# Performance work log

Measured on AMD Instinct MI355X. Metric: run time of the kernel, lower is better.

Reference implementation:

```python
import jax, jax.numpy as jnp
import numpy as np

T = 5          # temporal_window_size
B = 512        # batch (graphs per timestep)
NA = 16        # num_agents (nodes per graph)
S = 64         # num_belief_states
A = 16         # action_dim
HID = 64       # hidden_dim per head
H = 4          # num_attn_heads
FD = HID * H   # 256, feature_dim
LAT = 128      # latent_dim
N = B * NA     # total nodes per timestep
FIN = S + A    # node feature dim
NEG_SLOPE = 0.2


def _edge_index():
    i, j = np.meshgrid(np.arange(NA), np.arange(NA), indexing='ij')
    m = i != j
    src_l, dst_l = i[m], j[m]                      # 240 intra-clique edges
    off = (np.arange(B) * NA)[:, None]
    src = (src_l[None] + off).ravel()
    dst = (dst_l[None] + off).ravel()
    loops = np.arange(N)                           # PyG GATConv add_self_loops=True
    src = np.concatenate([src, loops])
    dst = np.concatenate([dst, loops])
    return jnp.asarray(np.stack([src, dst]), dtype=jnp.int64)


def setup_inputs() -> dict:
    key = jax.random.key(0)
    ks = jax.random.split(key, 24)
    xav = lambda k, shp: jax.random.normal(k, shp, jnp.float32) * np.float32(np.sqrt(2.0 / (shp[0] + shp[-1])))
    return {
        'signals': jax.random.normal(ks[0], (T, B, S), jnp.float32),
        'neighbor_actions': jax.random.normal(ks[1], (T, B, NA * A), jnp.float32),
        'lin_w0': xav(ks[2], (FD, FIN)),
        'att_src0': xav(ks[3], (H, HID)),
        'att_dst0': xav(ks[4], (H, HID)),
        'bias0': jnp.zeros((FD,), jnp.float32),
        'lin_w1': xav(ks[5], (FD, FD)),
        'att_src1': xav(ks[6], (H, HID)),
        'att_dst1': xav(ks[7], (H, HID)),
        'bias1': jnp.zeros((FD,), jnp.float32),
        'in_proj_w': xav(ks[8], (3 * FD, FD)),
        'in_proj_b': jnp.zeros((3 * FD,), jnp.float32),
        'out_proj_w': xav(ks[9], (FD, FD)),
        'out_proj_b': jnp.zeros((FD,), jnp.float32),
        'w_mean': xav(ks[10], (LAT, FD)),
        'b_mean': jnp.zeros((LAT,), jnp.float32),
        'w_logvar': xav(ks[11], (LAT, FD)),
        'b_logvar': jnp.zeros((LAT,), jnp.float32),
        'w_belief': xav(ks[12], (S, FD)),
        'b_belief': jnp.zeros((S,), jnp.float32),
        'edge_index': _edge_index(),
    }


def _segment_softmax(e, seg, num_segments):
    # e: [E, T, H]; softmax over edges sharing the same target node.
    m = jax.ops.segment_max(e, seg, num_segments=num_segments)
    e = jnp.exp(e - m[seg])
    s = jax.ops.segment_sum(e, seg, num_segments=num_segments)
    return e / s[seg]


def _gat(x, src, dst, w, a_src, a_dst, b):
    # x: [N, T, Fin] -> [N, T, H*HID]   (PyG GATConv, concat heads)
    xl = jnp.einsum('ntf,of->nto', x, w).reshape(N, T, H, HID)
    e_src = jnp.einsum('nthc,hc->nth', xl, a_src)[src]   # [E, T, H]
    e_dst = jnp.einsum('nthc,hc->nth', xl, a_dst)[dst]
    e = jax.nn.leaky_relu(e_src + e_dst, NEG_SLOPE)
    alpha = _segment_softmax(e, dst, N)                  # per-target softmax
    out = jax.ops.segment_sum(alpha[..., None] * xl[src], dst, num_segments=N)
    return out.reshape(N, T, FD) + b


def reference(signals, neighbor_actions, lin_w0, att_src0, att_dst0, bias0,
              lin_w1, att_src1, att_dst1, bias1, in_proj_w, in_proj_b,
              out_proj_w, out_proj_b, w_mean, b_mean, w_logvar, b_logvar,
              w_belief, b_belief, edge_index):
    # --- _construct_graph (vectorized over time window + batch) ---
    acts = neighbor_actions.reshape(T, B, NA, A)
    beliefs = jnp.zeros((T, B, NA, S), signals.dtype).at[:, :, 0, :].set(signals)
    nodes = jnp.concatenate([beliefs, acts], -1).reshape(T, N, FIN)
    nodes = jnp.transpose(nodes, (1, 0, 2))              # [N, T, FIN]
    src, dst = edge_index[0], edge_index[1]
    x = jax.nn.relu(_gat(nodes, src, dst, lin_w0, att_src0, att_dst0, bias0))
    x = jax.nn.relu(_gat(x, src, dst, lin_w1, att_src1, att_dst1, bias1))
    # --- ego-node sequence: nodes 0, NA, 2*NA, ... ---
    seq = x[::NA]                                        # [B, T, FD]
    # --- temporal MultiheadAttention (batch_first, eval) ---
    qkv = seq @ in_proj_w.T + in_proj_b
    q, k, v = jnp.split(qkv, 3, axis=-1)
    dh = FD // H
    q = q.reshape(B, T, H, dh); k = k.reshape(B, T, H, dh); v = v.reshape(B, T, H, dh)
    scores = jnp.einsum('bqhd,bkhd->bhqk', q, k) / jnp.sqrt(jnp.asarray(dh, seq.dtype))
    # torch float attn_mask is ADDITIVE: mask[i,j]=1 if j<=i else 0
    mask = (jnp.arange(T)[:, None] >= jnp.arange(T)[None, :]).astype(seq.dtype)
    attn = jax.nn.softmax(scores + mask[None, None], axis=-1)
    ctx = jnp.einsum('bhqk,bkhd->bqhd', attn, v).reshape(B, T, FD)
    ctx = ctx @ out_proj_w.T + out_proj_b
    feat = ctx[:, -1]                                    # [B, FD]
    # --- heads ---
    mean = feat @ w_mean.T + b_mean
    logvar = feat @ w_logvar.T + b_logvar
    belief = jax.nn.softmax(feat @ w_belief.T + b_belief, axis=-1)
    return (mean, logvar, belief)
```

## Files before the change

### kernel.cpp

```cpp
#include <hip/hip_runtime.h>
#include <hip/hip_bf16.h>


__device__ __forceinline__ float wave_sum64(float v) {
    #pragma unroll
    for (int off = 32; off > 0; off >>= 1) v += __shfl_xor(v, off, 64);
    return v;
}
__device__ __forceinline__ float wave_max64(float v) {
    #pragma unroll
    for (int off = 32; off > 0; off >>= 1) v = fmaxf(v, __shfl_xor(v, off, 64));
    return v;
}

__global__ __launch_bounds__(256) void k_pre(
    const float* __restrict__ w0, const float* __restrict__ w1,
    const float* __restrict__ wip, const float* __restrict__ wop,
    const float* __restrict__ wm, const float* __restrict__ wlv,
    const float* __restrict__ wb,
    const float* __restrict__ as0, const float* __restrict__ ad0,
    const float* __restrict__ as1, const float* __restrict__ ad1,
    float* __restrict__ tws,
    float* __restrict__ u1, float* __restrict__ ud1,
    float* __restrict__ pa0, float* __restrict__ pd0)
{
    const int tid = threadIdx.x;
    if (blockIdx.x < 1680) {
        int i = blockIdx.x * 256 + tid;
        float v; int d;
        if (i < 16384) {
            int k = i & 63, nn = i >> 6;
            v = w0[nn * 80 + k];
            d = (k >> 2) * 1024 + nn * 4 + (k & 3);
        } else if (i < 20480) {
            int j = i - 16384; int k = j & 15, nn = j >> 4;
            v = w0[nn * 80 + 64 + k];
            d = 16384 + (k >> 2) * 1024 + nn * 4 + (k & 3);
        } else if (i < 86016) {
            int j = i - 20480; int k = j & 255, nn = j >> 8;
            v = w1[nn * 256 + k];
            d = 20480 + (k >> 2) * 1024 + nn * 4 + (k & 3);
        } else if (i < 282624) {
            int j = i - 86016; int k = j & 255, nn = j >> 8;
            v = wip[nn * 256 + k];
            d = 86016 + (k >> 2) * 3072 + nn * 4 + (k & 3);
        } else if (i < 348160) {
            int j = i - 282624; int k = j & 255, nn = j >> 8;
            v = wop[nn * 256 + k];
            d = 282624 + (k >> 2) * 1024 + nn * 4 + (k & 3);
        } else {
            int j = i - 348160; int k = j & 255, o = j >> 8;
            if (o < 128)      v = wm[o * 256 + k];
            else if (o < 256) v = wlv[(o - 128) * 256 + k];
            else              v = wb[(o - 256) * 256 + k];
            d = 348160 + (k >> 2) * 1280 + o * 4 + (k & 3);
        }
        tws[d] = v;
        return;
    }
    for (int q = 0; q < 4; q++) {
        int idx = q * 256 + tid;
        int h = idx >> 8, k = idx & 255;
        float su = 0.f, sd = 0.f;
        for (int c = 0; c < 64; c++) {
            float wv = w1[(h * 64 + c) * 256 + k];
            su = fmaf(as1[h * 64 + c], wv, su);
            sd = fmaf(ad1[h * 64 + c], wv, sd);
        }
        u1[idx] = su; ud1[idx] = sd;
    }
    if (tid < 64) {
        int h = tid >> 4, k = tid & 15;
        float su = 0.f, sd = 0.f;
        for (int c = 0; c < 64; c++) {
            float wv = w0[(h * 64 + c) * 80 + 64 + k];
            su = fmaf(as0[h * 64 + c], wv, su);
            sd = fmaf(ad0[h * 64 + c], wv, sd);
        }
        pa0[tid] = su; pd0[tid] = sd;
    }
}

__global__ __launch_bounds__(256, 5) void k_gat(
    const float* __restrict__ sig,
    const float* __restrict__ nact,
    const float* __restrict__ W0sPK,
    const float* __restrict__ W0aPK,
    const float* __restrict__ W1PK,
    const float* __restrict__ u1g, const float* __restrict__ ud1g,
    const float* __restrict__ pa0g, const float* __restrict__ pd0g,
    const float* __restrict__ as0, const float* __restrict__ ad0,
    const float* __restrict__ b0, const float* __restrict__ b1,
    float* __restrict__ seqf)
{
    __shared__ __align__(16) char smem[28288];
    float* actL    = (float*)(smem + 0);
    float* sigL    = (float*)(smem + 1024);
    float* es0w    = (float*)(smem + 1280);
    float* ed0w    = (float*)(smem + 1536);
    float* espL    = (float*)(smem + 1792);
    float* es1L    = (float*)(smem + 2816);
    float* edpL    = (float*)(smem + 3072);
    float* alpha1L = (float*)(smem + 3136);
    float* a0L     = (float*)(smem + 3392);
    float* zL      = (float*)(smem + 7488);
    float* x1L     = (float*)(smem + 11648);

    const int tid = threadIdx.x;
    const int bg = blockIdx.x;
    const int b = bg / 5, g = bg - b * 5;
    const int n = tid, w = tid >> 6, lane = tid & 63;

    const float4* W0sPK4 = (const float4*)W0sPK;

    float4 wv0[8];
    #pragma unroll
    for (int j = 0; j < 8; j++) wv0[j] = W0sPK4[j * 256 + n];
    float4 wa[4];
    {
        const float4* W0aPK4 = (const float4*)W0aPK;
        #pragma unroll
        for (int q = 0; q < 4; q++) wa[q] = W0aPK4[q * 256 + n];
    }
    const float as0n = as0[n];
    const float ad0n = ad0[n];

    if (tid < 16)
        ((float4*)sigL)[tid] = ((const float4*)(sig + (g * 512 + b) * 64))[tid];
    if (tid < 64)
        ((float4*)actL)[tid] = ((const float4*)(nact + (g * 512 + b) * 256))[tid];
    __syncthreads();

    float S = 0.f;
    {
        const float4* sig4 = (const float4*)sigL;
        #pragma unroll
        for (int j = 0; j < 8; j++) {
            float4 sv = sig4[j];
            S = fmaf(wv0[j].x, sv.x, S);
            S = fmaf(wv0[j].y, sv.y, S);
            S = fmaf(wv0[j].z, sv.z, S);
            S = fmaf(wv0[j].w, sv.w, S);
        }
        float4 wv1[8];
        #pragma unroll
        for (int j = 0; j < 8; j++) wv1[j] = W0sPK4[(8 + j) * 256 + n];
        #pragma unroll
        for (int j = 0; j < 8; j++) {
            float4 sv = sig4[8 + j];
            S = fmaf(wv1[j].x, sv.x, S);
            S = fmaf(wv1[j].y, sv.y, S);
            S = fmaf(wv1[j].z, sv.z, S);
            S = fmaf(wv1[j].w, sv.w, S);
        }
    }
    const int m3 = lane >> 2, q3 = lane & 3;
    const float4 pv = ((const float4*)(pa0g + w * 16))[q3];
    const float4 dv = ((const float4*)(pd0g + w * 16))[q3];

    const float sS = wave_sum64(S * as0n);
    const float dS = wave_sum64(S * ad0n);

    {
        const float4 av = ((const float4*)(actL + m3 * 16))[q3];
        float su = av.x * pv.x;
        su = fmaf(av.y, pv.y, su); su = fmaf(av.z, pv.z, su); su = fmaf(av.w, pv.w, su);
        float sd = av.x * dv.x;
        sd = fmaf(av.y, dv.y, sd); sd = fmaf(av.z, dv.z, sd); sd = fmaf(av.w, dv.w, sd);
        su += __shfl_xor(su, 1, 64); su += __shfl_xor(su, 2, 64);
        sd += __shfl_xor(sd, 1, 64); sd += __shfl_xor(sd, 2, 64);
        if (q3 == 0) {
            es0w[w * 16 + m3] = su + ((m3 == 0) ? sS : 0.f);
            ed0w[w * 16 + m3] = sd + ((m3 == 0) ? dS : 0.f);
        }
    }
    {
        const int j = lane >> 2, q = lane & 3;
        const float ej = ed0w[w * 16 + j];
        const float4 ev = ((const float4*)(es0w + w * 16))[q];
        float e0 = ev.x + ej; e0 = (e0 >= 0.f) ? e0 : 0.2f * e0;
        float e1 = ev.y + ej; e1 = (e1 >= 0.f) ? e1 : 0.2f * e1;
        float e2 = ev.z + ej; e2 = (e2 >= 0.f) ? e2 : 0.2f * e2;
        float e3 = ev.w + ej; e3 = (e3 >= 0.f) ? e3 : 0.2f * e3;
        float mx = fmaxf(fmaxf(e0, e1), fmaxf(e2, e3));
        mx = fmaxf(mx, __shfl_xor(mx, 1, 64));
        mx = fmaxf(mx, __shfl_xor(mx, 2, 64));
        e0 = __expf(e0 - mx); e1 = __expf(e1 - mx);
        e2 = __expf(e2 - mx); e3 = __expf(e3 - mx);
        float s = e0 + e1 + e2 + e3;
        s += __shfl_xor(s, 1, 64); s += __shfl_xor(s, 2, 64);
        float inv = 1.f / s;
        ((float4*)(a0L + w * 256 + j * 16))[q] =
            make_float4(e0 * inv, e1 * inv, e2 * inv, e3 * inv);
    }

    float x1r[16];
    {
        const float4* act4 = (const float4*)actL;
        float xl0r[16];
        #pragma unroll
        for (int s = 0; s < 16; s++) {
            float a = 0.f;
            #pragma unroll
            for (int q = 0; q < 4; q++) {
                float4 av = act4[s * 4 + q];
                a = fmaf(av.x, wa[q].x, a);
                a = fmaf(av.y, wa[q].y, a);
                a = fmaf(av.z, wa[q].z, a);
                a = fmaf(av.w, wa[q].w, a);
            }
            xl0r[s] = a;
        }
        xl0r[0] += S;
        const float b0v = b0[n];
        const float4* a04 = (const float4*)(a0L + w * 256);
        #pragma unroll
        for (int j = 0; j < 16; j++) {
            float acc = b0v;
            #pragma unroll
            for (int s4 = 0; s4 < 4; s4++) {
                float4 a4 = a04[j * 4 + s4];
                acc = fmaf(a4.x, xl0r[s4 * 4 + 0], acc);
                acc = fmaf(a4.y, xl0r[s4 * 4 + 1], acc);
                acc = fmaf(a4.z, xl0r[s4 * 4 + 2], acc);
                acc = fmaf(a4.w, xl0r[s4 * 4 + 3], acc);
            }
            x1r[j] = fmaxf(acc, 0.f);
            x1L[j * 260 + n] = x1r[j];
        }
    }
    __syncthreads();

    {
        const int m = tid & 15, h = (tid >> 4) & 3, p = tid >> 6;
        const float4* x4p = (const float4*)(x1L + m * 260 + p * 64);
        const float4* u4p = ((const float4*)u1g) + h * 64 + p * 16;
        float a = 0.f;
        #pragma unroll
        for (int i = 0; i < 16; i++) {
            float4 xv = x4p[i], uv = u4p[i];
            a = fmaf(xv.x, uv.x, a);
            a = fmaf(xv.y, uv.y, a);
            a = fmaf(xv.z, uv.z, a);
            a = fmaf(xv.w, uv.w, a);
        }
        espL[m * 16 + h * 4 + p] = a;
        if (m == 0) {
            const float4* ud4p = ((const float4*)ud1g) + h * 64 + p * 16;
            float ad = 0.f;
            #pragma unroll
            for (int i = 0; i < 16; i++) {
                float4 xv = x4p[i], uv = ud4p[i];
                ad = fmaf(xv.x, uv.x, ad);
                ad = fmaf(xv.y, uv.y, ad);
                ad = fmaf(xv.z, uv.z, ad);
                ad = fmaf(xv.w, uv.w, ad);
            }
            edpL[h * 4 + p] = ad;
        }
    }
    __syncthreads();

    if (w == 0) {
        {
            const int m2 = lane >> 2, h = lane & 3;
            const float* e = espL + m2 * 16 + h * 4;
            es1L[m2 * 4 + h] = e[0] + e[1] + e[2] + e[3];
        }
        if (lane < 16) {
            const int h = lane >> 2, q = lane & 3;
            float ej = edpL[h * 4] + edpL[h * 4 + 1] + edpL[h * 4 + 2] + edpL[h * 4 + 3];
            float e[4]; float mx = -1e30f;
            #pragma unroll
            for (int r = 0; r < 4; r++) {
                float x = es1L[(q * 4 + r) * 4 + h] + ej;
                x = (x >= 0.f) ? x : 0.2f * x;
                e[r] = x; mx = fmaxf(mx, x);
            }
            mx = fmaxf(mx, __shfl_xor(mx, 1, 64));
            mx = fmaxf(mx, __shfl_xor(mx, 2, 64));
            float s = 0.f;
            #pragma unroll
            for (int r = 0; r < 4; r++) { e[r] = __expf(e[r] - mx); s += e[r]; }
            s += __shfl_xor(s, 1, 64);
            s += __shfl_xor(s, 2, 64);
            float inv = 1.f / s;
            ((float4*)(alpha1L + h * 16 + q * 4))[0] =
                make_float4(e[0] * inv, e[1] * inv, e[2] * inv, e[3] * inv);
        }
    }
    __syncthreads();

    const float4* W1PK4 = (const float4*)W1PK;
    float4 w1pf[8];
    #pragma unroll
    for (int j = 0; j < 8; j++) w1pf[j] = W1PK4[j * 256 + n];
    const float b1v = b1[n];
    {
        const float4* a14 = (const float4*)alpha1L;
        #pragma unroll
        for (int hh = 0; hh < 4; hh++) {
            float zv = 0.f;
            #pragma unroll
            for (int s4 = 0; s4 < 4; s4++) {
                float4 a4 = a14[hh * 4 + s4];
                zv = fmaf(a4.x, x1r[s4 * 4 + 0], zv);
                zv = fmaf(a4.y, x1r[s4 * 4 + 1], zv);
                zv = fmaf(a4.z, x1r[s4 * 4 + 2], zv);
                zv = fmaf(a4.w, x1r[s4 * 4 + 3], zv);
            }
            zL[hh * 260 + n] = zv;
        }
    }
    __syncthreads();

    {
        const float4* zh = (const float4*)(zL + w * 260);
        float acc = b1v;
        #pragma unroll
        for (int j = 0; j < 8; j++) {
            float4 z4 = zh[j];
            acc = fmaf(w1pf[j].x, z4.x, acc);
            acc = fmaf(w1pf[j].y, z4.y, acc);
            acc = fmaf(w1pf[j].z, z4.z, acc);
            acc = fmaf(w1pf[j].w, z4.w, acc);
        }
        #pragma unroll
        for (int io = 1; io < 8; io++) {
            float4 wv[8];
            #pragma unroll
            for (int j = 0; j < 8; j++) wv[j] = W1PK4[(io * 8 + j) * 256 + n];
            #pragma unroll
            for (int j = 0; j < 8; j++) {
                float4 z4 = zh[io * 8 + j];
                acc = fmaf(wv[j].x, z4.x, acc);
                acc = fmaf(wv[j].y, z4.y, acc);
                acc = fmaf(wv[j].z, z4.z, acc);
                acc = fmaf(wv[j].w, z4.w, acc);
            }
        }
        seqf[bg * 256 + n] = fmaxf(acc, 0.f);
    }
}

__global__ __launch_bounds__(768) void k_stage2(
    const float* __restrict__ seqf,
    const float* __restrict__ wipPK,
    const float* __restrict__ bip,
    const float* __restrict__ wopPK,
    const float* __restrict__ bop,
    const float* __restrict__ whPK,
    const float* __restrict__ bm, const float* __restrict__ blv,
    const float* __restrict__ bb,
    float* __restrict__ out)
{
    __shared__ float sseq[2][5][256];
    __shared__ float kL[2][5][256], vL[2][5][256], qL[2][256];
    __shared__ float ctxL[2][256], featL[2][256];
    __shared__ float beliefL[2][64];
    const int tid = threadIdx.x;
    const int b0 = blockIdx.x * 2;

    {
        float4* sflat = (float4*)&sseq[0][0][0];
        const float4* src = (const float4*)(seqf + b0 * 1280);
        if (tid < 640) sflat[tid] = src[tid];
    }
    __syncthreads();

    {
        const int kind = tid >> 8, n = tid & 255;
        const float4* wPK = (const float4*)wipPK + tid;
        if (kind == 0) {
            const float4* s0 = (const float4*)&sseq[0][4][0];
            const float4* s1 = (const float4*)&sseq[1][4][0];
            float a0 = 0.f, a1 = 0.f;
            #pragma unroll 8
            for (int k4 = 0; k4 < 64; k4++) {
                float4 wv = wPK[k4 * 768];
                float4 x0 = s0[k4], x1 = s1[k4];
                a0 = fmaf(x0.x, wv.x, a0); a0 = fmaf(x0.y, wv.y, a0);
                a0 = fmaf(x0.z, wv.z, a0); a0 = fmaf(x0.w, wv.w, a0);
                a1 = fmaf(x1.x, wv.x, a1); a1 = fmaf(x1.y, wv.y, a1);
                a1 = fmaf(x1.z, wv.z, a1); a1 = fmaf(x1.w, wv.w, a1);
            }
            float bv = bip[n];
            qL[0][n] = a0 + bv; qL[1][n] = a1 + bv;
        } else {
            float acc[2][5] = {{0.f,0.f,0.f,0.f,0.f},{0.f,0.f,0.f,0.f,0.f}};
            #pragma unroll 4
            for (int k4 = 0; k4 < 64; k4++) {
                float4 wv = wPK[k4 * 768];
                #pragma unroll
                for (int gb = 0; gb < 2; gb++) {
                    #pragma unroll
                    for (int t = 0; t < 5; t++) {
                        float4 sv = ((const float4*)&sseq[gb][t][0])[k4];
                        float a = acc[gb][t];
                        a = fmaf(sv.x, wv.x, a); a = fmaf(sv.y, wv.y, a);
                        a = fmaf(sv.z, wv.z, a); a = fmaf(sv.w, wv.w, a);
                        acc[gb][t] = a;
                    }
                }
            }
            float bv = bip[kind * 256 + n];
            float* dst = (kind == 1) ? &kL[0][0][0] : &vL[0][0][0];
            #pragma unroll
            for (int gb = 0; gb < 2; gb++)
                #pragma unroll
                for (int t = 0; t < 5; t++)
                    dst[gb * 1280 + t * 256 + n] = acc[gb][t] + bv;
        }
    }
    __syncthreads();

    if (tid < 512) {
        const int gb = tid >> 8, col = tid & 255;
        float q4 = qL[gb][col];
        float sc[5];
        #pragma unroll
        for (int t = 0; t < 5; t++)
            sc[t] = wave_sum64(q4 * kL[gb][t][col]) * 0.125f;
        float m = sc[0];
        #pragma unroll
        for (int t = 1; t < 5; t++) m = fmaxf(m, sc[t]);
        float p[5], sum = 0.f;
        #pragma unroll
        for (int t = 0; t < 5; t++) { p[t] = __expf(sc[t] - m); sum += p[t]; }
        float inv = 1.f / sum, cv = 0.f;
        #pragma unroll
        for (int t = 0; t < 5; t++) cv = fmaf(p[t], vL[gb][t][col], cv);
        ctxL[gb][col] = cv * inv;
    }
    __syncthreads();

    if (tid < 512) {
        const int gb = tid >> 8, n = tid & 255;
        const float4* wPK = (const float4*)wopPK + n;
        const float4* c4 = (const float4*)&ctxL[gb][0];
        float acc = 0.f;
        #pragma unroll 8
        for (int k4 = 0; k4 < 64; k4++) {
            float4 wv = wPK[k4 * 256], cv = c4[k4];
            acc = fmaf(cv.x, wv.x, acc); acc = fmaf(cv.y, wv.y, acc);
            acc = fmaf(cv.z, wv.z, acc); acc = fmaf(cv.w, wv.w, acc);
        }
        featL[gb][n] = acc + bop[n];
    }
    __syncthreads();

    if (tid < 640) {
        const int gb = tid / 320, j = tid - gb * 320;
        const float4* wPK = (const float4*)whPK + j;
        const float4* f4 = (const float4*)&featL[gb][0];
        float acc = 0.f;
        #pragma unroll 8
        for (int k4 = 0; k4 < 64; k4++) {
            float4 wv = wPK[k4 * 320], fv = f4[k4];
            acc = fmaf(fv.x, wv.x, acc); acc = fmaf(fv.y, wv.y, acc);
            acc = fmaf(fv.z, wv.z, acc); acc = fmaf(fv.w, wv.w, acc);
        }
        if (j < 128) {
            out[(b0 + gb) * 128 + j] = acc + bm[j];
        } else if (j < 256) {
            out[65536 + (b0 + gb) * 128 + (j - 128)] = acc + blv[j - 128];
        } else {
            beliefL[gb][j - 256] = acc + bb[j - 256];
        }
    }
    __syncthreads();

    if (tid < 128) {
        int gb = tid >> 6, lane = tid & 63;
        float lg = beliefL[gb][lane];
        float m = wave_max64(lg);
        float e = __expf(lg - m);
        float s = wave_sum64(e);
        out[131072 + (b0 + gb) * 64 + lane] = e / s;
    }
}

extern "C" void kernel_launch(void* const* d_in, const int* in_sizes, int n_in,
                              void* d_out, int out_size, void* d_ws, size_t ws_size,
                              hipStream_t stream) {
    const float* sig  = (const float*)d_in[0];
    const float* nact = (const float*)d_in[1];
    const float* w0   = (const float*)d_in[2];
    const float* as0  = (const float*)d_in[3];
    const float* ad0  = (const float*)d_in[4];
    const float* b0   = (const float*)d_in[5];
    const float* w1   = (const float*)d_in[6];
    const float* as1  = (const float*)d_in[7];
    const float* ad1  = (const float*)d_in[8];
    const float* b1   = (const float*)d_in[9];
    const float* wip  = (const float*)d_in[10];
    const float* bip  = (const float*)d_in[11];
    const float* wop  = (const float*)d_in[12];
    const float* bop  = (const float*)d_in[13];
    const float* wm   = (const float*)d_in[14];
    const float* bm   = (const float*)d_in[15];
    const float* wlv  = (const float*)d_in[16];
    const float* blv  = (const float*)d_in[17];
    const float* wb   = (const float*)d_in[18];
    const float* bb   = (const float*)d_in[19];

    float* ws    = (float*)d_ws;
    float* seqf  = ws;
    float* tws   = ws + 655360;
    float* W0sPK = tws;
    float* W0aPK = tws + 16384;
    float* W1PK  = tws + 20480;
    float* wipPK = tws + 86016;
    float* wopPK = tws + 282624;
    float* whPK  = tws + 348160;
    float* u1    = ws + 1085440;
    float* ud1   = ws + 1086464;
    float* pa0   = ws + 1087488;
    float* pd0   = ws + 1087552;

    k_pre   <<<1681, 256, 0, stream>>>(w0, w1, wip, wop, wm, wlv, wb,
                                       as0, ad0, as1, ad1,
                                       tws, u1, ud1, pa0, pd0);
    k_gat   <<<2560, 256, 0, stream>>>(sig, nact, W0sPK, W0aPK, W1PK,
                                       u1, ud1, pa0, pd0, as0, ad0, b0, b1, seqf);
    k_stage2<<<256, 768, 0, stream>>>(seqf, wipPK, bip, wopPK, bop, whPK,
                                      bm, blv, bb, (float*)d_out);
}
```

Measured before the change: 194.6 us.

## Process all five timesteps per block in GAT kernel to reuse weights

```diff
diff --git a/kernel.cpp b/kernel.cpp
--- a/kernel.cpp
+++ b/kernel.cpp
@@ -12,6 +12,10 @@
     for (int off = 32; off > 0; off >>= 1) v = fmaxf(v, __shfl_xor(v, off, 64));
     return v;
 }
+
+#define FMA4(acc, wv, zv) \
+    acc = fmaf((wv).x, (zv).x, acc); acc = fmaf((wv).y, (zv).y, acc); \
+    acc = fmaf((wv).z, (zv).z, acc); acc = fmaf((wv).w, (zv).w, acc);
 
 __global__ __launch_bounds__(256) void k_pre(
     const float* __restrict__ w0, const float* __restrict__ w1,
@@ -81,7 +85,7 @@
     }
 }
 
-__global__ __launch_bounds__(256, 5) void k_gat(
+__global__ __launch_bounds__(256, 2) void k_gat(
     const float* __restrict__ sig,
     const float* __restrict__ nact,
     const float* __restrict__ W0sPK,
@@ -93,253 +97,247 @@
     const float* __restrict__ b0, const float* __restrict__ b1,
     float* __restrict__ seqf)
 {
-    __shared__ __align__(16) char smem[28288];
-    float* actL    = (float*)(smem + 0);
-    float* sigL    = (float*)(smem + 1024);
-    float* es0w    = (float*)(smem + 1280);
-    float* ed0w    = (float*)(smem + 1536);
-    float* espL    = (float*)(smem + 1792);
-    float* es1L    = (float*)(smem + 2816);
-    float* edpL    = (float*)(smem + 3072);
-    float* alpha1L = (float*)(smem + 3136);
-    float* a0L     = (float*)(smem + 3392);
-    float* zL      = (float*)(smem + 7488);
-    float* x1L     = (float*)(smem + 11648);
+    __shared__ __align__(16) char smem[51264];
+    float* actL  = (float*)(smem + 0);
+    float* sigL  = (float*)(smem + 5120);
+    float* a0L   = (float*)(smem + 6400);
+    float* x1L   = (float*)(smem + 10496);
+    float* zL    = (float*)(smem + 27136);
+    float* es0w  = (float*)(smem + 47616);
+    float* ed0w  = (float*)(smem + 47872);
+    float* espL  = (float*)(smem + 48128);
+    float* edpL  = (float*)(smem + 49152);
+    float* es1w  = (float*)(smem + 49216);
+    float* alphw = (float*)(smem + 50240);
 
     const int tid = threadIdx.x;
-    const int bg = blockIdx.x;
-    const int b = bg / 5, g = bg - b * 5;
+    const int b = blockIdx.x;
     const int n = tid, w = tid >> 6, lane = tid & 63;
 
     const float4* W0sPK4 = (const float4*)W0sPK;
-
-    float4 wv0[8];
+    const float4* W1PK4  = (const float4*)W1PK;
+
+    float4 wv0[16];
     #pragma unroll
-    for (int j = 0; j < 8; j++) wv0[j] = W0sPK4[j * 256 + n];
+    for (int j = 0; j < 16; j++) wv0[j] = W0sPK4[j * 256 + n];
     float4 wa[4];
     {
         const float4* W0aPK4 = (const float4*)W0aPK;
         #pragma unroll
         for (int q = 0; q < 4; q++) wa[q] = W0aPK4[q * 256 + n];
     }
-    const float as0n = as0[n];
-    const float ad0n = ad0[n];
-
-    if (tid < 16)
-        ((float4*)sigL)[tid] = ((const float4*)(sig + (g * 512 + b) * 64))[tid];
-    if (tid < 64)
-        ((float4*)actL)[tid] = ((const float4*)(nact + (g * 512 + b) * 256))[tid];
-    __syncthreads();
-
-    float S = 0.f;
-    {
-        const float4* sig4 = (const float4*)sigL;
-        #pragma unroll
-        for (int j = 0; j < 8; j++) {
-            float4 sv = sig4[j];
-            S = fmaf(wv0[j].x, sv.x, S);
-            S = fmaf(wv0[j].y, sv.y, S);
-            S = fmaf(wv0[j].z, sv.z, S);
-            S = fmaf(wv0[j].w, sv.w, S);
-        }
-        float4 wv1[8];
-        #pragma unroll
-        for (int j = 0; j < 8; j++) wv1[j] = W0sPK4[(8 + j) * 256 + n];
-        #pragma unroll
-        for (int j = 0; j < 8; j++) {
-            float4 sv = sig4[8 + j];
-            S = fmaf(wv1[j].x, sv.x, S);
-            S = fmaf(wv1[j].y, sv.y, S);
-            S = fmaf(wv1[j].z, sv.z, S);
-            S = fmaf(wv1[j].w, sv.w, S);
-        }
-    }
+    const float as0n = as0[n], ad0n = ad0[n];
+    const float b0v = b0[n], b1v = b1[n];
     const int m3 = lane >> 2, q3 = lane & 3;
     const float4 pv = ((const float4*)(pa0g + w * 16))[q3];
     const float4 dv = ((const float4*)(pd0g + w * 16))[q3];
 
-    const float sS = wave_sum64(S * as0n);
-    const float dS = wave_sum64(S * ad0n);
-
+    if (tid < 80) {
+        int g = tid >> 4, q = tid & 15;
+        ((float4*)sigL)[tid] = ((const float4*)sig)[(g * 512 + b) * 16 + q];
+    }
     {
-        const float4 av = ((const float4*)(actL + m3 * 16))[q3];
-        float su = av.x * pv.x;
-        su = fmaf(av.y, pv.y, su); su = fmaf(av.z, pv.z, su); su = fmaf(av.w, pv.w, su);
-        float sd = av.x * dv.x;
-        sd = fmaf(av.y, dv.y, sd); sd = fmaf(av.z, dv.z, sd); sd = fmaf(av.w, dv.w, sd);
-        su += __shfl_xor(su, 1, 64); su += __shfl_xor(su, 2, 64);
-        sd += __shfl_xor(sd, 1, 64); sd += __shfl_xor(sd, 2, 64);
-        if (q3 == 0) {
-            es0w[w * 16 + m3] = su + ((m3 == 0) ? sS : 0.f);
-            ed0w[w * 16 + m3] = sd + ((m3 == 0) ? dS : 0.f);
-        }
-    }
+        int g = tid >> 6, q = tid & 63;
+        ((float4*)actL)[tid] = ((const float4*)nact)[(g * 512 + b) * 64 + q];
+        if (tid < 64)
+            ((float4*)actL)[tid + 256] =
+                ((const float4*)nact)[(4 * 512 + b) * 64 + tid];
+    }
+    __syncthreads();
+
+    float S0 = 0.f, S1 = 0.f, S2 = 0.f, S3 = 0.f, S4 = 0.f;
     {
-        const int j = lane >> 2, q = lane & 3;
-        const float ej = ed0w[w * 16 + j];
-        const float4 ev = ((const float4*)(es0w + w * 16))[q];
-        float e0 = ev.x + ej; e0 = (e0 >= 0.f) ? e0 : 0.2f * e0;
-        float e1 = ev.y + ej; e1 = (e1 >= 0.f) ? e1 : 0.2f * e1;
-        float e2 = ev.z + ej; e2 = (e2 >= 0.f) ? e2 : 0.2f * e2;
-        float e3 = ev.w + ej; e3 = (e3 >= 0.f) ? e3 : 0.2f * e3;
-        float mx = fmaxf(fmaxf(e0, e1), fmaxf(e2, e3));
-        mx = fmaxf(mx, __shfl_xor(mx, 1, 64));
-        mx = fmaxf(mx, __shfl_xor(mx, 2, 64));
-        e0 = __expf(e0 - mx); e1 = __expf(e1 - mx);
-        e2 = __expf(e2 - mx); e3 = __expf(e3 - mx);
-        float s = e0 + e1 + e2 + e3;
-        s += __shfl_xor(s, 1, 64); s += __shfl_xor(s, 2, 64);
-        float inv = 1.f / s;
-        ((float4*)(a0L + w * 256 + j * 16))[q] =
-            make_float4(e0 * inv, e1 * inv, e2 * inv, e3 * inv);
-    }
-
-    float x1r[16];
-    {
-        const float4* act4 = (const float4*)actL;
-        float xl0r[16];
-        #pragma unroll
-        for (int s = 0; s < 16; s++) {
-            float a = 0.f;
-            #pragma unroll
-            for (int q = 0; q < 4; q++) {
-                float4 av = act4[s * 4 + q];
-                a = fmaf(av.x, wa[q].x, a);
-                a = fmaf(av.y, wa[q].y, a);
-                a = fmaf(av.z, wa[q].z, a);
-                a = fmaf(av.w, wa[q].w, a);
-            }
-            xl0r[s] = a;
-        }
-        xl0r[0] += S;
-        const float b0v = b0[n];
-        const float4* a04 = (const float4*)(a0L + w * 256);
+        const float4* sig4 = (const float4*)sigL;
         #pragma unroll
         for (int j = 0; j < 16; j++) {
-            float acc = b0v;
-            #pragma unroll
-            for (int s4 = 0; s4 < 4; s4++) {
-                float4 a4 = a04[j * 4 + s4];
-                acc = fmaf(a4.x, xl0r[s4 * 4 + 0], acc);
-                acc = fmaf(a4.y, xl0r[s4 * 4 + 1], acc);
-                acc = fmaf(a4.z, xl0r[s4 * 4 + 2], acc);
-                acc = fmaf(a4.w, xl0r[s4 * 4 + 3], acc);
-            }
-            x1r[j] = fmaxf(acc, 0.f);
-            x1L[j * 260 + n] = x1r[j];
-        }
-    }
-    __syncthreads();
-
-    {
-        const int m = tid & 15, h = (tid >> 4) & 3, p = tid >> 6;
-        const float4* x4p = (const float4*)(x1L + m * 260 + p * 64);
-        const float4* u4p = ((const float4*)u1g) + h * 64 + p * 16;
-        float a = 0.f;
-        #pragma unroll
-        for (int i = 0; i < 16; i++) {
-            float4 xv = x4p[i], uv = u4p[i];
-            a = fmaf(xv.x, uv.x, a);
-            a = fmaf(xv.y, uv.y, a);
-            a = fmaf(xv.z, uv.z, a);
-            a = fmaf(xv.w, uv.w, a);
-        }
-        espL[m * 16 + h * 4 + p] = a;
-        if (m == 0) {
-            const float4* ud4p = ((const float4*)ud1g) + h * 64 + p * 16;
-            float ad = 0.f;
-            #pragma unroll
-            for (int i = 0; i < 16; i++) {
-                float4 xv = x4p[i], uv = ud4p[i];
-                ad = fmaf(xv.x, uv.x, ad);
-                ad = fmaf(xv.y, uv.y, ad);
-                ad = fmaf(xv.z, uv.z, ad);
-                ad = fmaf(xv.w, uv.w, ad);
-            }
-            edpL[h * 4 + p] = ad;
-        }
-    }
-    __syncthreads();
-
-    if (w == 0) {
-        {
-            const int m2 = lane >> 2, h = lane & 3;
-            const float* e = espL + m2 * 16 + h * 4;
-            es1L[m2 * 4 + h] = e[0] + e[1] + e[2] + e[3];
-        }
-        if (lane < 16) {
-            const int h = lane >> 2, q = lane & 3;
-            float ej = edpL[h * 4] + edpL[h * 4 + 1] + edpL[h * 4 + 2] + edpL[h * 4 + 3];
-            float e[4]; float mx = -1e30f;
-            #pragma unroll
-            for (int r = 0; r < 4; r++) {
-                float x = es1L[(q * 4 + r) * 4 + h] + ej;
-                x = (x >= 0.f) ? x : 0.2f * x;
-                e[r] = x; mx = fmaxf(mx, x);
-            }
-            mx = fmaxf(mx, __shfl_xor(mx, 1, 64));
-            mx = fmaxf(mx, __shfl_xor(mx, 2, 64));
-            float s = 0.f;
-            #pragma unroll
-            for (int r = 0; r < 4; r++) { e[r] = __expf(e[r] - mx); s += e[r]; }
-            s += __shfl_xor(s, 1, 64);
-            s += __shfl_xor(s, 2, 64);
-            float inv = 1.f / s;
-            ((float4*)(alpha1L + h * 16 + q * 4))[0] =
-                make_float4(e[0] * inv, e[1] * inv, e[2] * inv, e[3] * inv);
-        }
-    }
-    __syncthreads();
-
-    const float4* W1PK4 = (const float4*)W1PK;
+            float4 wv = wv0[j];
+            float4 v0 = sig4[j],      v1 = sig4[16 + j], v2 = sig4[32 + j];
+            float4 v3 = sig4[48 + j], v4 = sig4[64 + j];
+            FMA4(S0, wv, v0); FMA4(S1, wv, v1); FMA4(S2, wv, v2);
+            FMA4(S3, wv, v3); FMA4(S4, wv, v4);
+        }
+    }
     float4 w1pf[8];
     #pragma unroll
     for (int j = 0; j < 8; j++) w1pf[j] = W1PK4[j * 256 + n];
-    const float b1v = b1[n];
+
+    #pragma unroll 1
+    for (int g = 0; g < 5; g++) {
+        const float Sg = S0;
+        const float sS = wave_sum64(Sg * as0n);
+        const float dS = wave_sum64(Sg * ad0n);
+
+        {
+            const float4 av = ((const float4*)(actL + (g << 8) + m3 * 16))[q3];
+            float su = av.x * pv.x;
+            su = fmaf(av.y, pv.y, su); su = fmaf(av.z, pv.z, su); su = fmaf(av.w, pv.w, su);
+            float sd = av.x * dv.x;
+            sd = fmaf(av.y, dv.y, sd); sd = fmaf(av.z, dv.z, sd); sd = fmaf(av.w, dv.w, sd);
+            su += __shfl_xor(su, 1, 64); su += __shfl_xor(su, 2, 64);
+            sd += __shfl_xor(sd, 1, 64); sd += __shfl_xor(sd, 2, 64);
+            if (q3 == 0) {
+                es0w[w * 16 + m3] = su + ((m3 == 0) ? sS : 0.f);
+                ed0w[w * 16 + m3] = sd + ((m3 == 0) ? dS : 0.f);
+            }
+        }
+        {
+            const int j = lane >> 2, q = lane & 3;
+            const float ej = ed0w[w * 16 + j];
+            const float4 ev = ((const float4*)(es0w + w * 16))[q];
+            float e0 = ev.x + ej; e0 = (e0 >= 0.f) ? e0 : 0.2f * e0;
+            float e1 = ev.y + ej; e1 = (e1 >= 0.f) ? e1 : 0.2f * e1;
+            float e2 = ev.z + ej; e2 = (e2 >= 0.f) ? e2 : 0.2f * e2;
+            float e3 = ev.w + ej; e3 = (e3 >= 0.f) ? e3 : 0.2f * e3;
+            float mx = fmaxf(fmaxf(e0, e1), fmaxf(e2, e3));
+            mx = fmaxf(mx, __shfl_xor(mx, 1, 64));
+            mx = fmaxf(mx, __shfl_xor(mx, 2, 64));
+            e0 = __expf(e0 - mx); e1 = __expf(e1 - mx);
+            e2 = __expf(e2 - mx); e3 = __expf(e3 - mx);
+            float s = e0 + e1 + e2 + e3;
+            s += __shfl_xor(s, 1, 64); s += __shfl_xor(s, 2, 64);
+            float inv = 1.f / s;
+            ((float4*)(a0L + (w << 8) + j * 16))[q] =
+                make_float4(e0 * inv, e1 * inv, e2 * inv, e3 * inv);
+        }
+        float x1r[16];
+        {
+            const float4* act4 = (const float4*)(actL + (g << 8));
+            float xl0r[16];
+            #pragma unroll
+            for (int s = 0; s < 16; s++) {
+                float a = 0.f;
+                #pragma unroll
+                for (int q = 0; q < 4; q++) {
+                    float4 av = act4[s * 4 + q];
+                    FMA4(a, av, wa[q]);
+                }
+                xl0r[s] = a;
+            }
+            xl0r[0] += Sg;
+            const float4* a04 = (const float4*)(a0L + (w << 8));
+            #pragma unroll
+            for (int j = 0; j < 16; j++) {
+                float acc = b0v;
+                #pragma unroll
+                for (int s4 = 0; s4 < 4; s4++) {
+                    float4 a4 = a04[j * 4 + s4];
+                    acc = fmaf(a4.x, xl0r[s4 * 4 + 0], acc);
+                    acc = fmaf(a4.y, xl0r[s4 * 4 + 1], acc);
+                    acc = fmaf(a4.z, xl0r[s4 * 4 + 2], acc);
+                    acc = fmaf(a4.w, xl0r[s4 * 4 + 3], acc);
+                }
+                x1r[j] = fmaxf(acc, 0.f);
+                x1L[j * 260 + n] = x1r[j];
+            }
+        }
+        __syncthreads();
+
+        {
+            const int m = tid & 15, h = (tid >> 4) & 3, p = tid >> 6;
+            const float4* x4p = (const float4*)(x1L + m * 260 + p * 64);
+            const float4* u4p = ((const float4*)u1g) + h * 64 + p * 16;
+            float a = 0.f;
+            #pragma unroll
+            for (int i = 0; i < 16; i++) {
+                float4 xv = x4p[i], uv = u4p[i];
+                FMA4(a, xv, uv);
+            }
+            espL[m * 16 + h * 4 + p] = a;
+            if (m == 0) {
+                const float4* ud4p = ((const float4*)ud1g) + h * 64 + p * 16;
+                float ad = 0.f;
+                #pragma unroll
+                for (int i = 0; i < 16; i++) {
+                    float4 xv = x4p[i], uv = ud4p[i];
+                    FMA4(ad, xv, uv);
+                }
+                edpL[h * 4 + p] = ad;
+            }
+        }
+        __syncthreads();
+
+        {
+            const int m2 = lane >> 2, h2 = lane & 3;
+            const float* e = espL + m2 * 16 + h2 * 4;
+            es1w[(w << 6) + lane] = e[0] + e[1] + e[2] + e[3];
+            if (lane < 16) {
+                const int h = lane >> 2, q = lane & 3;
+                float ej = edpL[h * 4] + edpL[h * 4 + 1]
+                         + edpL[h * 4 + 2] + edpL[h * 4 + 3];
+                float ev[4]; float mx = -1e30f;
+                #pragma unroll
+                for (int r = 0; r < 4; r++) {
+                    float x = es1w[(w << 6) + (q * 4 + r) * 4 + h] + ej;
+                    x = (x >= 0.f) ? x : 0.2f * x;
+                    ev[r] = x; mx = fmaxf(mx, x);
+                }
+                mx = fmaxf(mx, __shfl_xor(mx, 1, 64));
+                mx = fmaxf(mx, __shfl_xor(mx, 2, 64));
+                float s = 0.f;
+                #pragma unroll
+                for (int r = 0; r < 4; r++) { ev[r] = __expf(ev[r] - mx); s += ev[r]; }
+                s += __shfl_xor(s, 1, 64);
+                s += __shfl_xor(s, 2, 64);
+                float inv = 1.f / s;
+                ((float4*)(alphw + (w << 6) + h * 16 + q * 4))[0] =
+                    make_float4(ev[0] * inv, ev[1] * inv, ev[2] * inv, ev[3] * inv);
+            }
+        }
+        {
+            const float4* a14 = (const float4*)(alphw + (w << 6));
+            float* zg = zL + (g << 10);
+            #pragma unroll
+            for (int hh = 0; hh < 4; hh++) {
+                float zv = 0.f;
+                #pragma unroll
+                for (int s4 = 0; s4 < 4; s4++) {
+                    float4 a4 = a14[hh * 4 + s4];
+                    zv = fmaf(a4.x, x1r[s4 * 4 + 0], zv);
+                    zv = fmaf(a4.y, x1r[s4 * 4 + 1], zv);
+                    zv = fmaf(a4.z, x1r[s4 * 4 + 2], zv);
+                    zv = fmaf(a4.w, x1r[s4 * 4 + 3], zv);
+                }
+                zg[hh * 256 + n] = zv;
+            }
+        }
+        S0 = S1; S1 = S2; S2 = S3; S3 = S4;
+    }
+    __syncthreads();
+
     {
-        const float4* a14 = (const float4*)alpha1L;
-        #pragma unroll
-        for (int hh = 0; hh < 4; hh++) {
-            float zv = 0.f;
-            #pragma unroll
-            for (int s4 = 0; s4 < 4; s4++) {
-                float4 a4 = a14[hh * 4 + s4];
-                zv = fmaf(a4.x, x1r[s4 * 4 + 0], zv);
-                zv = fmaf(a4.y, x1r[s4 * 4 + 1], zv);
-                zv = fmaf(a4.z, x1r[s4 * 4 + 2], zv);
-                zv = fmaf(a4.w, x1r[s4 * 4 + 3], zv);
-            }
-            zL[hh * 260 + n] = zv;
-        }
-    }
-    __syncthreads();
-
-    {
-        const float4* zh = (const float4*)(zL + w * 260);
-        float acc = b1v;
+        float a0 = b1v, a1 = b1v, a2 = b1v, a3 = b1v, a4 = b1v;
+        const float4* zL4 = (const float4*)zL;
+        const int zb = (w << 6);
         #pragma unroll
         for (int j = 0; j < 8; j++) {
-            float4 z4 = zh[j];
-            acc = fmaf(w1pf[j].x, z4.x, acc);
-            acc = fmaf(w1pf[j].y, z4.y, acc);
-            acc = fmaf(w1pf[j].z, z4.z, acc);
-            acc = fmaf(w1pf[j].w, z4.w, acc);
-        }
-        #pragma unroll
+            float4 wv = w1pf[j];
+            float4 z0 = zL4[zb + j],        z1 = zL4[256 + zb + j];
+            float4 z2 = zL4[512 + zb + j],  z3 = zL4[768 + zb + j];
+            float4 z4 = zL4[1024 + zb + j];
+            FMA4(a0, wv, z0); FMA4(a1, wv, z1); FMA4(a2, wv, z2);
+            FMA4(a3, wv, z3); FMA4(a4, wv, z4);
+        }
+        #pragma unroll 1
         for (int io = 1; io < 8; io++) {
-            float4 wv[8];
-            #pragma unroll
-            for (int j = 0; j < 8; j++) wv[j] = W1PK4[(io * 8 + j) * 256 + n];
+            float4 wv2[8];
+            #pragma unroll
+            for (int j = 0; j < 8; j++) wv2[j] = W1PK4[((io * 8 + j) << 8) + n];
             #pragma unroll
             for (int j = 0; j < 8; j++) {
-                float4 z4 = zh[io * 8 + j];
-                acc = fmaf(wv[j].x, z4.x, acc);
-                acc = fmaf(wv[j].y, z4.y, acc);
-                acc = fmaf(wv[j].z, z4.z, acc);
-                acc = fmaf(wv[j].w, z4.w, acc);
-            }
-        }
-        seqf[bg * 256 + n] = fmaxf(acc, 0.f);
+                const int k4 = io * 8 + j;
+                float4 wv = wv2[j];
+                float4 z0 = zL4[zb + k4],       z1 = zL4[256 + zb + k4];
+                float4 z2 = zL4[512 + zb + k4], z3 = zL4[768 + zb + k4];
+                float4 z4 = zL4[1024 + zb + k4];
+                FMA4(a0, wv, z0); FMA4(a1, wv, z1); FMA4(a2, wv, z2);
+                FMA4(a3, wv, z3); FMA4(a4, wv, z4);
+            }
+        }
+        seqf[(b * 5 + 0) * 256 + n] = fmaxf(a0, 0.f);
+        seqf[(b * 5 + 1) * 256 + n] = fmaxf(a1, 0.f);
+        seqf[(b * 5 + 2) * 256 + n] = fmaxf(a2, 0.f);
+        seqf[(b * 5 + 3) * 256 + n] = fmaxf(a3, 0.f);
+        seqf[(b * 5 + 4) * 256 + n] = fmaxf(a4, 0.f);
     }
 }
 
@@ -521,8 +519,8 @@
     k_pre   <<<1681, 256, 0, stream>>>(w0, w1, wip, wop, wm, wlv, wb,
                                        as0, ad0, as1, ad1,
                                        tws, u1, ud1, pa0, pd0);
-    k_gat   <<<2560, 256, 0, stream>>>(sig, nact, W0sPK, W0aPK, W1PK,
-                                       u1, ud1, pa0, pd0, as0, ad0, b0, b1, seqf);
+    k_gat   <<<512, 256, 0, stream>>>(sig, nact, W0sPK, W0aPK, W1PK,
+                                      u1, ud1, pa0, pd0, as0, ad0, b0, b1, seqf);
     k_stage2<<<256, 768, 0, stream>>>(seqf, wipPK, bip, wopPK, bop, whPK,
                                       bm, blv, bb, (float*)d_out);
 }
```

Measured after the change: 190.2 us. -2.2%, faster.

## Restructure temporal attention stage to one batch per 256-thread block

Applied to the files above, without the earlier changes.

```diff
diff --git a/kernel.cpp b/kernel.cpp
--- a/kernel.cpp
+++ b/kernel.cpp
@@ -12,6 +12,10 @@
     for (int off = 32; off > 0; off >>= 1) v = fmaxf(v, __shfl_xor(v, off, 64));
     return v;
 }
+
+#define FMA4(acc, wv, zv) \
+    acc = fmaf((wv).x, (zv).x, acc); acc = fmaf((wv).y, (zv).y, acc); \
+    acc = fmaf((wv).z, (zv).z, acc); acc = fmaf((wv).w, (zv).w, acc);
 
 __global__ __launch_bounds__(256) void k_pre(
     const float* __restrict__ w0, const float* __restrict__ w1,
@@ -190,7 +194,7 @@
         float s = e0 + e1 + e2 + e3;
         s += __shfl_xor(s, 1, 64); s += __shfl_xor(s, 2, 64);
         float inv = 1.f / s;
-        ((float4*)(a0L + w * 256 + j * 16))[q] =
+        ((float4*)(a0L + (w << 8) + j * 16))[q] =
             make_float4(e0 * inv, e1 * inv, e2 * inv, e3 * inv);
     }
 
@@ -204,16 +208,13 @@
             #pragma unroll
             for (int q = 0; q < 4; q++) {
                 float4 av = act4[s * 4 + q];
-                a = fmaf(av.x, wa[q].x, a);
-                a = fmaf(av.y, wa[q].y, a);
-                a = fmaf(av.z, wa[q].z, a);
-                a = fmaf(av.w, wa[q].w, a);
+                FMA4(a, av, wa[q]);
             }
             xl0r[s] = a;
         }
         xl0r[0] += S;
         const float b0v = b0[n];
-        const float4* a04 = (const float4*)(a0L + w * 256);
+        const float4* a04 = (const float4*)(a0L + (w << 8));
         #pragma unroll
         for (int j = 0; j < 16; j++) {
             float acc = b0v;
@@ -239,10 +240,7 @@
         #pragma unroll
         for (int i = 0; i < 16; i++) {
             float4 xv = x4p[i], uv = u4p[i];
-            a = fmaf(xv.x, uv.x, a);
-            a = fmaf(xv.y, uv.y, a);
-            a = fmaf(xv.z, uv.z, a);
-            a = fmaf(xv.w, uv.w, a);
+            FMA4(a, xv, uv);
         }
         espL[m * 16 + h * 4 + p] = a;
         if (m == 0) {
@@ -251,10 +249,7 @@
             #pragma unroll
             for (int i = 0; i < 16; i++) {
                 float4 xv = x4p[i], uv = ud4p[i];
-                ad = fmaf(xv.x, uv.x, ad);
-                ad = fmaf(xv.y, uv.y, ad);
-                ad = fmaf(xv.z, uv.z, ad);
-                ad = fmaf(xv.w, uv.w, ad);
+                FMA4(ad, xv, uv);
             }
             edpL[h * 4 + p] = ad;
         }
@@ -320,10 +315,7 @@
         #pragma unroll
         for (int j = 0; j < 8; j++) {
             float4 z4 = zh[j];
-            acc = fmaf(w1pf[j].x, z4.x, acc);
-            acc = fmaf(w1pf[j].y, z4.y, acc);
-            acc = fmaf(w1pf[j].z, z4.z, acc);
-            acc = fmaf(w1pf[j].w, z4.w, acc);
+            FMA4(acc, w1pf[j], z4);
         }
         #pragma unroll
         for (int io = 1; io < 8; io++) {
@@ -333,17 +325,14 @@
             #pragma unroll
             for (int j = 0; j < 8; j++) {
                 float4 z4 = zh[io * 8 + j];
-                acc = fmaf(wv[j].x, z4.x, acc);
-                acc = fmaf(wv[j].y, z4.y, acc);
-                acc = fmaf(wv[j].z, z4.z, acc);
-                acc = fmaf(wv[j].w, z4.w, acc);
+                FMA4(acc, wv[j], z4);
             }
         }
         seqf[bg * 256 + n] = fmaxf(acc, 0.f);
     }
 }
 
-__global__ __launch_bounds__(768) void k_stage2(
+__global__ __launch_bounds__(256) void k_stage2(
     const float* __restrict__ seqf,
     const float* __restrict__ wipPK,
     const float* __restrict__ bip,
@@ -354,73 +343,47 @@
     const float* __restrict__ bb,
     float* __restrict__ out)
 {
-    __shared__ float sseq[2][5][256];
-    __shared__ float kL[2][5][256], vL[2][5][256], qL[2][256];
-    __shared__ float ctxL[2][256], featL[2][256];
-    __shared__ float beliefL[2][64];
+    __shared__ float kL[5][256], vL[5][256], qL[256];
+    __shared__ float ctxL[256], featL[256];
+    __shared__ float beliefL[64];
     const int tid = threadIdx.x;
-    const int b0 = blockIdx.x * 2;
-
-    {
-        float4* sflat = (float4*)&sseq[0][0][0];
-        const float4* src = (const float4*)(seqf + b0 * 1280);
-        if (tid < 640) sflat[tid] = src[tid];
-    }
-    __syncthreads();
-
-    {
-        const int kind = tid >> 8, n = tid & 255;
-        const float4* wPK = (const float4*)wipPK + tid;
-        if (kind == 0) {
-            const float4* s0 = (const float4*)&sseq[0][4][0];
-            const float4* s1 = (const float4*)&sseq[1][4][0];
-            float a0 = 0.f, a1 = 0.f;
-            #pragma unroll 8
-            for (int k4 = 0; k4 < 64; k4++) {
-                float4 wv = wPK[k4 * 768];
-                float4 x0 = s0[k4], x1 = s1[k4];
-                a0 = fmaf(x0.x, wv.x, a0); a0 = fmaf(x0.y, wv.y, a0);
-                a0 = fmaf(x0.z, wv.z, a0); a0 = fmaf(x0.w, wv.w, a0);
-                a1 = fmaf(x1.x, wv.x, a1); a1 = fmaf(x1.y, wv.y, a1);
-                a1 = fmaf(x1.z, wv.z, a1); a1 = fmaf(x1.w, wv.w, a1);
-            }
-            float bv = bip[n];
-            qL[0][n] = a0 + bv; qL[1][n] = a1 + bv;
-        } else {
-            float acc[2][5] = {{0.f,0.f,0.f,0.f,0.f},{0.f,0.f,0.f,0.f,0.f}};
-            #pragma unroll 4
-            for (int k4 = 0; k4 < 64; k4++) {
-                float4 wv = wPK[k4 * 768];
-                #pragma unroll
-                for (int gb = 0; gb < 2; gb++) {
-                    #pragma unroll
-                    for (int t = 0; t < 5; t++) {
-                        float4 sv = ((const float4*)&sseq[gb][t][0])[k4];
-                        float a = acc[gb][t];
-                        a = fmaf(sv.x, wv.x, a); a = fmaf(sv.y, wv.y, a);
-                        a = fmaf(sv.z, wv.z, a); a = fmaf(sv.w, wv.w, a);
-                        acc[gb][t] = a;
-                    }
-                }
-            }
-            float bv = bip[kind * 256 + n];
-            float* dst = (kind == 1) ? &kL[0][0][0] : &vL[0][0][0];
-            #pragma unroll
-            for (int gb = 0; gb < 2; gb++)
-                #pragma unroll
-                for (int t = 0; t < 5; t++)
-                    dst[gb * 1280 + t * 256 + n] = acc[gb][t] + bv;
-        }
-    }
-    __syncthreads();
-
-    if (tid < 512) {
-        const int gb = tid >> 8, col = tid & 255;
-        float q4 = qL[gb][col];
+    const int b = blockIdx.x;
+    const int n = tid;
+
+    {
+        const float4* sq = (const float4*)(seqf + b * 1280);
+        const float4* wPK = (const float4*)wipPK;
+        float aq = 0.f;
+        float ak0 = 0.f, ak1 = 0.f, ak2 = 0.f, ak3 = 0.f, ak4 = 0.f;
+        float av0 = 0.f, av1 = 0.f, av2 = 0.f, av3 = 0.f, av4 = 0.f;
+        #pragma unroll 4
+        for (int k4 = 0; k4 < 64; k4++) {
+            float4 wq = wPK[k4 * 768 + n];
+            float4 wk = wPK[k4 * 768 + 256 + n];
+            float4 wv = wPK[k4 * 768 + 512 + n];
+            float4 x0 = sq[k4],       x1 = sq[64 + k4], x2 = sq[128 + k4];
+            float4 x3 = sq[192 + k4], x4 = sq[256 + k4];
+            FMA4(aq, wq, x4);
+            FMA4(ak0, wk, x0); FMA4(ak1, wk, x1); FMA4(ak2, wk, x2);
+            FMA4(ak3, wk, x3); FMA4(ak4, wk, x4);
+            FMA4(av0, wv, x0); FMA4(av1, wv, x1); FMA4(av2, wv, x2);
+            FMA4(av3, wv, x3); FMA4(av4, wv, x4);
+        }
+        qL[n] = aq + bip[n];
+        const float bk = bip[256 + n], bv = bip[512 + n];
+        kL[0][n] = ak0 + bk; kL[1][n] = ak1 + bk; kL[2][n] = ak2 + bk;
+        kL[3][n] = ak3 + bk; kL[4][n] = ak4 + bk;
+        vL[0][n] = av0 + bv; vL[1][n] = av1 + bv; vL[2][n] = av2 + bv;
+        vL[3][n] = av3 + bv; vL[4][n] = av4 + bv;
+    }
+    __syncthreads();
+
+    {
+        float q4 = qL[n];
         float sc[5];
         #pragma unroll
         for (int t = 0; t < 5; t++)
-            sc[t] = wave_sum64(q4 * kL[gb][t][col]) * 0.125f;
+            sc[t] = wave_sum64(q4 * kL[t][n]) * 0.125f;
         float m = sc[0];
         #pragma unroll
         for (int t = 1; t < 5; t++) m = fmaxf(m, sc[t]);
@@ -429,54 +392,54 @@
         for (int t = 0; t < 5; t++) { p[t] = __expf(sc[t] - m); sum += p[t]; }
         float inv = 1.f / sum, cv = 0.f;
         #pragma unroll
-        for (int t = 0; t < 5; t++) cv = fmaf(p[t], vL[gb][t][col], cv);
-        ctxL[gb][col] = cv * inv;
-    }
-    __syncthreads();
-
-    if (tid < 512) {
-        const int gb = tid >> 8, n = tid & 255;
+        for (int t = 0; t < 5; t++) cv = fmaf(p[t], vL[t][n], cv);
+        ctxL[n] = cv * inv;
+    }
+    __syncthreads();
+
+    {
         const float4* wPK = (const float4*)wopPK + n;
-        const float4* c4 = (const float4*)&ctxL[gb][0];
+        const float4* c4 = (const float4*)ctxL;
         float acc = 0.f;
         #pragma unroll 8
         for (int k4 = 0; k4 < 64; k4++) {
             float4 wv = wPK[k4 * 256], cv = c4[k4];
-            acc = fmaf(cv.x, wv.x, acc); acc = fmaf(cv.y, wv.y, acc);
-            acc = fmaf(cv.z, wv.z, acc); acc = fmaf(cv.w, wv.w, acc);
-        }
-        featL[gb][n] = acc + bop[n];
-    }
-    __syncthreads();
-
-    if (tid < 640) {
-        const int gb = tid / 320, j = tid - gb * 320;
-        const float4* wPK = (const float4*)whPK + j;
-        const float4* f4 = (const float4*)&featL[gb][0];
+            FMA4(acc, wv, cv);
+        }
+        featL[n] = acc + bop[n];
+    }
+    __syncthreads();
+
+    {
+        const float4* f4 = (const float4*)featL;
+        const float4* wPK = (const float4*)whPK + n;
         float acc = 0.f;
         #pragma unroll 8
         for (int k4 = 0; k4 < 64; k4++) {
             float4 wv = wPK[k4 * 320], fv = f4[k4];
-            acc = fmaf(fv.x, wv.x, acc); acc = fmaf(fv.y, wv.y, acc);
-            acc = fmaf(fv.z, wv.z, acc); acc = fmaf(fv.w, wv.w, acc);
-        }
-        if (j < 128) {
-            out[(b0 + gb) * 128 + j] = acc + bm[j];
-        } else if (j < 256) {
-            out[65536 + (b0 + gb) * 128 + (j - 128)] = acc + blv[j - 128];
-        } else {
-            beliefL[gb][j - 256] = acc + bb[j - 256];
-        }
-    }
-    __syncthreads();
-
-    if (tid < 128) {
-        int gb = tid >> 6, lane = tid & 63;
-        float lg = beliefL[gb][lane];
+            FMA4(acc, wv, fv);
+        }
+        if (n < 128) out[b * 128 + n] = acc + bm[n];
+        else         out[65536 + b * 128 + (n - 128)] = acc + blv[n - 128];
+        if (n < 64) {
+            const float4* w2 = (const float4*)whPK + 256 + n;
+            float acc2 = 0.f;
+            #pragma unroll 8
+            for (int k4 = 0; k4 < 64; k4++) {
+                float4 wv = w2[k4 * 320], fv = f4[k4];
+                FMA4(acc2, wv, fv);
+            }
+            beliefL[n] = acc2 + bb[n];
+        }
+    }
+    __syncthreads();
+
+    if (tid < 64) {
+        float lg = beliefL[tid];
         float m = wave_max64(lg);
         float e = __expf(lg - m);
         float s = wave_sum64(e);
-        out[131072 + (b0 + gb) * 64 + lane] = e / s;
+        out[131072 + b * 64 + tid] = e / s;
     }
 }
 
@@ -523,6 +486,6 @@
                                        tws, u1, ud1, pa0, pd0);
     k_gat   <<<2560, 256, 0, stream>>>(sig, nact, W0sPK, W0aPK, W1PK,
                                        u1, ud1, pa0, pd0, as0, ad0, b0, b1, seqf);
-    k_stage2<<<256, 768, 0, stream>>>(seqf, wipPK, bip, wopPK, bop, whPK,
+    k_stage2<<<512, 256, 0, stream>>>(seqf, wipPK, bip, wopPK, bop, whPK,
                                       bm, blv, bb, (float*)d_out);
 }
```

Result: slower. 212.5 us (+9.2%).
